# Performance work log

Measured on AMD Instinct MI355X. Metric: run time of the kernel, lower is better.

## Reference

```python
import jax, jax.numpy as jnp
import numpy as np

ANNEAL = 0.01
N, D, NUM_CLASSES = 384, 128, 24


def setup_inputs() -> dict:
    key = jax.random.key(0)
    k1, k2 = jax.random.split(key)
    preds = jax.random.normal(k1, (N, D), dtype=jnp.float32)
    # L2-normalize embeddings (standard for SmoothAP cosine similarities)
    preds = preds / jnp.linalg.norm(preds, axis=1, keepdims=True)
    labels = jax.random.randint(k2, (N,), 0, NUM_CLASSES, dtype=jnp.int64)
    return {"preds": preds, "labels": labels}


def reference(preds, labels):
    n = preds.shape[0]
    dt = preds.dtype
    eye = jnp.eye(n, dtype=dt)
    # I_pos[i,j] = 1 iff same label and i != j (lmu.get_all_pairs_indices)
    I_pos = (labels[:, None] == labels[None, :]).astype(dt) * (1 - eye)
    sim = preds @ preds.T                              # [N, N]
    # sim_diff[a,b,c] = sim[a,c] - sim[a,b]  (unsqueeze(1) - unsqueeze(2))
    diff = sim[:, None, :] - sim[:, :, None]           # [N, N, N]
    sg = jax.nn.sigmoid(jnp.clip(diff / ANNEAL, -50.0, 50.0))
    sg = sg * (1 - eye)                                # zero where b == c
    # sum_c sg[a,b,c] * I_pos[a,c], then gate by I_pos[a,b]
    pos_sum = jnp.einsum('abc,ac->ab', sg, I_pos) * I_pos
    sim_pos_rk = 1 + I_pos + pos_sum                   # [N, N]
    sim_all_rk = 1 + jnp.sum(sg, axis=-1)              # [N, N]
    n_pos = jnp.sum(I_pos, axis=1) + 1                 # [N]
    per_i = jnp.sum(sim_pos_rk / sim_all_rk, axis=1) / n_pos
    ap = jnp.sum(jnp.where(n_pos > 1, per_i, jnp.zeros((), dt))) / n
    return (1 - ap)[None]                              # shape (1,), like torch
```

## Files before the change

kernel.cpp:

```cpp
#include <hip/hip_runtime.h>

#define N 384
#define D 128

__device__ const float KLOG2E = 144.26950408889634f;
__device__ const float ECLAMP = 72.13475204444817f;

__global__ __launch_bounds__(N) void smoothap_main(const float* __restrict__ preds,
                                                   const int* __restrict__ labels,
                                                   float* __restrict__ per_a) {
    __shared__ float4 s_pa[D / 4];
    __shared__ float2 s_sp[N];
    __shared__ int    s_lab[N];
    __shared__ float  s_red[12];

    const int a = blockIdx.x;
    const int t = threadIdx.x;

    if (t < D / 4) s_pa[t] = ((const float4*)(preds + (size_t)a * D))[t];
    s_lab[t] = labels[t];
    __syncthreads();

    const float4* pt = (const float4*)(preds + (size_t)t * D);
    float acc = 0.f;
#pragma unroll
    for (int k = 0; k < D / 4; ++k) {
        float4 v = pt[k];
        float4 w = s_pa[k];
        acc = fmaf(v.x, w.x, acc);
        acc = fmaf(v.y, w.y, acc);
        acc = fmaf(v.z, w.z, acc);
        acc = fmaf(v.w, w.w, acc);
    }
    const int la = s_lab[a];
    const float posf = (s_lab[t] == la && t != a) ? 1.f : 0.f;
    s_sp[t] = make_float2(acc, posf);
    __syncthreads();

    const float simab = acc;
    const float mab = simab * KLOG2E;

    float all_sum = 0.f;
    float pos_sum = 0.f;
    const float4* sp4 = (const float4*)s_sp;
#pragma unroll 4
    for (int j = 0; j < N / 2; ++j) {
        float4 q = sp4[j];
        float e0 = fmaf(q.x, -KLOG2E, mab);
        e0 = fminf(fmaxf(e0, -ECLAMP), ECLAMP);
        float sg0 = __builtin_amdgcn_rcpf(1.f + __builtin_amdgcn_exp2f(e0));
        float e1 = fmaf(q.z, -KLOG2E, mab);
        e1 = fminf(fmaxf(e1, -ECLAMP), ECLAMP);
        float sg1 = __builtin_amdgcn_rcpf(1.f + __builtin_amdgcn_exp2f(e1));
        all_sum += sg0 + sg1;
        pos_sum = fmaf(sg0, q.y, pos_sum);
        pos_sum = fmaf(sg1, q.w, pos_sum);
    }
    all_sum -= 0.5f;
    pos_sum -= 0.5f * posf;

    const float ratio = fmaf(posf, 1.f + pos_sum, 1.f) / (1.f + all_sum);

    const int lane = t & 63;
    const int wid = t >> 6;
    float r = ratio;
    float np = posf;
#pragma unroll
    for (int off = 32; off; off >>= 1) {
        r += __shfl_down(r, off);
        np += __shfl_down(np, off);
    }
    if (lane == 0) {
        s_red[wid] = r;
        s_red[6 + wid] = np;
    }
    __syncthreads();
    if (t == 0) {
        float rs = 0.f, ns = 0.f;
#pragma unroll
        for (int w = 0; w < 6; ++w) {
            rs += s_red[w];
            ns += s_red[6 + w];
        }
        const float n_pos = ns + 1.f;
        per_a[a] = (ns > 0.5f) ? (rs / n_pos) : 0.f;
    }
}

__global__ __launch_bounds__(N) void smoothap_final(const float* __restrict__ per_a,
                                                    float* __restrict__ out) {
    __shared__ float s_red[6];
    const int t = threadIdx.x;
    float v = per_a[t];
    const int lane = t & 63;
    const int wid = t >> 6;
#pragma unroll
    for (int off = 32; off; off >>= 1) v += __shfl_down(v, off);
    if (lane == 0) s_red[wid] = v;
    __syncthreads();
    if (t == 0) {
        float s = 0.f;
#pragma unroll
        for (int w = 0; w < 6; ++w) s += s_red[w];
        out[0] = 1.f - s / (float)N;
    }
}

extern "C" void kernel_launch(void* const* d_in, const int* in_sizes, int n_in,
                              void* d_out, int out_size, void* d_ws, size_t ws_size,
                              hipStream_t stream) {
    const float* preds = (const float*)d_in[0];
    const int* labels = (const int*)d_in[1];
    float* out = (float*)d_out;
    float* per_a = (float*)d_ws;

    smoothap_main<<<N, N, 0, stream>>>(preds, labels, per_a);
    smoothap_final<<<1, N, 0, stream>>>(per_a, out);
}
```

Before: 89.54 us.

## Fuse final reduction via atomics and split inner loop across two thread halves

Merges the two kernels into one, with the final mean accumulated into the output through a per-block atomicAdd after a memset. Each block now runs 768 threads, so two threads split the 384-term sigmoid sum for each (a,b) pair, and the partial sums are combined through shared memory. The exp-argument clamps are also dropped. This removes one kernel launch and raises parallelism per block, at the cost of an extra memset, an extra barrier and a non-deterministic order of the float atomic sums.

```diff
diff --git a/kernel.cpp b/kernel.cpp
--- a/kernel.cpp
+++ b/kernel.cpp
@@ -1,70 +1,78 @@
 #include <hip/hip_runtime.h>
 
 #define N 384
-#define D 128
+#define NT 768
+#define HALF_ITERS 96
 
 __device__ const float KLOG2E = 144.26950408889634f;
-__device__ const float ECLAMP = 72.13475204444817f;
 
-__global__ __launch_bounds__(N) void smoothap_main(const float* __restrict__ preds,
-                                                   const int* __restrict__ labels,
-                                                   float* __restrict__ per_a) {
-    __shared__ float4 s_pa[D / 4];
-    __shared__ float2 s_sp[N];
-    __shared__ int    s_lab[N];
-    __shared__ float  s_red[12];
+__global__ __launch_bounds__(NT) void smoothap_fused(const float* __restrict__ preds,
+                                                     const int* __restrict__ labels,
+                                                     float* __restrict__ out) {
+    __shared__ __align__(16) float4 s_pa[32];
+    __shared__ __align__(16) float2 s_sp[N];
+    __shared__ __align__(16) float2 s_part[N];
+    __shared__ int   s_lab[N];
+    __shared__ float s_red[24];
 
     const int a = blockIdx.x;
     const int t = threadIdx.x;
+    const int half = (t >= N) ? 1 : 0;
+    const int b = t - half * N;
 
-    if (t < D / 4) s_pa[t] = ((const float4*)(preds + (size_t)a * D))[t];
-    s_lab[t] = labels[t];
+    if (t < N) s_lab[t] = labels[t];
+    if (t < 32) s_pa[t] = ((const float4*)(preds + (size_t)a * 128))[t];
     __syncthreads();
 
-    const float4* pt = (const float4*)(preds + (size_t)t * D);
-    float acc = 0.f;
+    if (t < N) {
+        const float4* pt = (const float4*)(preds + (size_t)t * 128);
+        float acc = 0.f;
 #pragma unroll
-    for (int k = 0; k < D / 4; ++k) {
-        float4 v = pt[k];
-        float4 w = s_pa[k];
-        acc = fmaf(v.x, w.x, acc);
-        acc = fmaf(v.y, w.y, acc);
-        acc = fmaf(v.z, w.z, acc);
-        acc = fmaf(v.w, w.w, acc);
+        for (int k = 0; k < 32; ++k) {
+            float4 v = pt[k];
+            float4 w = s_pa[k];
+            acc = fmaf(v.x, w.x, acc);
+            acc = fmaf(v.y, w.y, acc);
+            acc = fmaf(v.z, w.z, acc);
+            acc = fmaf(v.w, w.w, acc);
+        }
+        const float posf = (s_lab[t] == s_lab[a] && t != a) ? 1.f : 0.f;
+        s_sp[t] = make_float2(acc, posf);
     }
-    const int la = s_lab[a];
-    const float posf = (s_lab[t] == la && t != a) ? 1.f : 0.f;
-    s_sp[t] = make_float2(acc, posf);
     __syncthreads();
 
-    const float simab = acc;
-    const float mab = simab * KLOG2E;
+    const float2 me = s_sp[b];
+    const float mab = me.x * KLOG2E;
+    const float posf = me.y;
 
-    float all_sum = 0.f;
-    float pos_sum = 0.f;
+    float all_sum = 0.f, pos_sum = 0.f;
     const float4* sp4 = (const float4*)s_sp;
+    const int j0 = half * HALF_ITERS;
 #pragma unroll 4
-    for (int j = 0; j < N / 2; ++j) {
+    for (int j = j0; j < j0 + HALF_ITERS; ++j) {
         float4 q = sp4[j];
         float e0 = fmaf(q.x, -KLOG2E, mab);
-        e0 = fminf(fmaxf(e0, -ECLAMP), ECLAMP);
         float sg0 = __builtin_amdgcn_rcpf(1.f + __builtin_amdgcn_exp2f(e0));
         float e1 = fmaf(q.z, -KLOG2E, mab);
-        e1 = fminf(fmaxf(e1, -ECLAMP), ECLAMP);
         float sg1 = __builtin_amdgcn_rcpf(1.f + __builtin_amdgcn_exp2f(e1));
         all_sum += sg0 + sg1;
         pos_sum = fmaf(sg0, q.y, pos_sum);
         pos_sum = fmaf(sg1, q.w, pos_sum);
     }
-    all_sum -= 0.5f;
-    pos_sum -= 0.5f * posf;
+    if (half) s_part[b] = make_float2(all_sum, pos_sum);
+    __syncthreads();
 
-    const float ratio = fmaf(posf, 1.f + pos_sum, 1.f) / (1.f + all_sum);
+    float r = 0.f, np = 0.f;
+    if (t < N) {
+        const float2 o = s_part[b];
+        const float all = all_sum + o.x - 0.5f;
+        const float pos = pos_sum + o.y - 0.5f * posf;
+        r = fmaf(posf, 1.f + pos, 1.f) / (1.f + all);
+        np = posf;
+    }
 
     const int lane = t & 63;
     const int wid = t >> 6;
-    float r = ratio;
-    float np = posf;
 #pragma unroll
     for (int off = 32; off; off >>= 1) {
         r += __shfl_down(r, off);
@@ -72,37 +80,19 @@
     }
     if (lane == 0) {
         s_red[wid] = r;
-        s_red[6 + wid] = np;
+        s_red[12 + wid] = np;
     }
     __syncthreads();
     if (t == 0) {
         float rs = 0.f, ns = 0.f;
 #pragma unroll
-        for (int w = 0; w < 6; ++w) {
+        for (int w = 0; w < 12; ++w) {
             rs += s_red[w];
-            ns += s_red[6 + w];
+            ns += s_red[12 + w];
         }
-        const float n_pos = ns + 1.f;
-        per_a[a] = (ns > 0.5f) ? (rs / n_pos) : 0.f;
-    }
-}
-
-__global__ __launch_bounds__(N) void smoothap_final(const float* __restrict__ per_a,
-                                                    float* __restrict__ out) {
-    __shared__ float s_red[6];
-    const int t = threadIdx.x;
-    float v = per_a[t];
-    const int lane = t & 63;
-    const int wid = t >> 6;
-#pragma unroll
-    for (int off = 32; off; off >>= 1) v += __shfl_down(v, off);
-    if (lane == 0) s_red[wid] = v;
-    __syncthreads();
-    if (t == 0) {
-        float s = 0.f;
-#pragma unroll
-        for (int w = 0; w < 6; ++w) s += s_red[w];
-        out[0] = 1.f - s / (float)N;
+        const float per_i = (ns > 0.5f) ? rs / (ns + 1.f) : 0.f;
+        const float contrib = fmaf(per_i, -1.f / (float)N, (a == 0) ? 1.f : 0.f);
+        atomicAdd(out, contrib);
     }
 }
 
@@ -112,8 +102,7 @@
     const float* preds = (const float*)d_in[0];
     const int* labels = (const int*)d_in[1];
     float* out = (float*)d_out;
-    float* per_a = (float*)d_ws;
 
-    smoothap_main<<<N, N, 0, stream>>>(preds, labels, per_a);
-    smoothap_final<<<1, N, 0, stream>>>(per_a, out);
+    hipMemsetAsync(out, 0, sizeof(float), stream);
+    smoothap_fused<<<N, NT, 0, stream>>>(preds, labels, out);
 }
```

Result: faster. 82.74 us (-7.6%).
